# Performance work log

Hardware: AMD Instinct MI355X
Metric: run time of the kernel (lower is better)

The kernel has to match this reference:

```python
import jax, jax.numpy as jnp
import numpy as np

B, L, N, D = 128, 256, 64, 1024  # batch, text_len, img_num, feat size (text=obj=place=D)


def masked_softmax(logits, mask=None):
    # matches MaskedSoftmax(dim=1): softmax over last axis, then renormalize by mask
    dist = jax.nn.softmax(logits, axis=-1)
    if mask is None:
        return dist
    dist = dist * mask
    return dist / jnp.sum(dist, axis=-1, keepdims=True)


def setup_inputs() -> dict:
    key = jax.random.key(0)
    ks = jax.random.split(key, 32)
    s = lambda d: 1.0 / np.sqrt(d)
    inp = {
        'text_feat': jax.random.normal(ks[0], (B, D), jnp.float32),
        'text_feats': jax.random.normal(ks[1], (B, L, D), jnp.float32),
        'img_object_feat': jax.random.normal(ks[2], (B, D), jnp.float32),
        'img_object_feats': jax.random.normal(ks[3], (B, N, D), jnp.float32),
        'img_place_feat': jax.random.normal(ks[4], (B, D), jnp.float32),
        'img_place_feats': jax.random.normal(ks[5], (B, N, D), jnp.float32),
        'src_mask': (jax.random.uniform(ks[6], (B, L)) < 0.9).astype(jnp.float32).at[:, 0].set(1.0),
        # score vectors (nn.Linear(D,1,bias=False))
        'v_to': jax.random.uniform(ks[7], (D,), jnp.float32, -s(D), s(D)),
        'v_tp': jax.random.uniform(ks[8], (D,), jnp.float32, -s(D), s(D)),
        'v_io': jax.random.uniform(ks[9], (D,), jnp.float32, -s(D), s(D)),
        'v_ip': jax.random.uniform(ks[10], (D,), jnp.float32, -s(D), s(D)),
        # cross-modal projections (bias=False), torch layout [out,in]
        'W_t2o': jax.random.uniform(ks[11], (D, D), jnp.float32, -s(D), s(D)),
        'W_t2p': jax.random.uniform(ks[12], (D, D), jnp.float32, -s(D), s(D)),
        'W_o2t': jax.random.uniform(ks[13], (D, D), jnp.float32, -s(D), s(D)),
        'W_p2t': jax.random.uniform(ks[14], (D, D), jnp.float32, -s(D), s(D)),
        # self projections with bias
        'W_oo': jax.random.uniform(ks[15], (D, D), jnp.float32, -s(D), s(D)),
        'b_oo': jax.random.uniform(ks[16], (D,), jnp.float32, -s(D), s(D)),
        'W_pp': jax.random.uniform(ks[17], (D, D), jnp.float32, -s(D), s(D)),
        'b_pp': jax.random.uniform(ks[18], (D,), jnp.float32, -s(D), s(D)),
        'W_tot': jax.random.uniform(ks[19], (D, D), jnp.float32, -s(D), s(D)),
        'b_tot': jax.random.uniform(ks[20], (D,), jnp.float32, -s(D), s(D)),
        'W_tpt': jax.random.uniform(ks[21], (D, D), jnp.float32, -s(D), s(D)),
        'b_tpt': jax.random.uniform(ks[22], (D,), jnp.float32, -s(D), s(D)),
        # output linear: in = 2*D + D + D = 4D
        'W_out': jax.random.uniform(ks[23], (D, 4 * D), jnp.float32, -s(4 * D), s(4 * D)),
        'b_out': jax.random.uniform(ks[24], (D,), jnp.float32, -s(4 * D), s(4 * D)),
    }
    return inp


def _text_att_ctx(text_feat, img_feats, W_img2text, W_text, b_text, v):
    # additive attention of text over image regions
    e = jnp.tanh(jnp.einsum('bnd,td->bnt', img_feats, W_img2text)
                 + (text_feat @ W_text.T + b_text)[:, None, :])
    scores = jnp.einsum('bnt,t->bn', e, v)
    dist = masked_softmax(scores)
    return jnp.einsum('bn,bnd->bd', dist, img_feats)


def _img_att_ctx(img_feat, text_feats, W_text2img, W_img, b_img, v, mask):
    e = jnp.tanh(jnp.einsum('bld,id->bli', text_feats, W_text2img)
                 + (img_feat @ W_img.T + b_img)[:, None, :])
    scores = jnp.einsum('bli,i->bl', e, v)
    dist = masked_softmax(scores, mask)
    return jnp.einsum('bl,bld->bd', dist, text_feats)


def reference(text_feat, text_feats, img_object_feat, img_object_feats, img_place_feat,
              img_place_feats, src_mask, v_to, v_tp, v_io, v_ip, W_t2o, W_t2p, W_o2t,
              W_p2t, W_oo, b_oo, W_pp, b_pp, W_tot, b_tot, W_tpt, b_tpt, W_out, b_out):
    img_object_context = _text_att_ctx(text_feat, img_object_feats, W_o2t, W_tot, b_tot, v_to)
    img_place_context = _text_att_ctx(text_feat, img_place_feats, W_p2t, W_tpt, b_tpt, v_tp)
    text_object_context = _img_att_ctx(img_object_feat, text_feats, W_t2o, W_oo, b_oo, v_io, src_mask)
    text_place_context = _img_att_ctx(img_place_feat, text_feats, W_t2p, W_pp, b_pp, v_ip, src_mask)
    combined = jnp.concatenate([img_object_context, img_place_context,
                                text_object_context, text_place_context], axis=1)
    # dropout is identity at inference
    return combined @ W_out.T + b_out
```

## Files before the change

### kernel.cpp

```cpp
#include <hip/hip_runtime.h>
#include <hip/hip_bf16.h>

typedef __attribute__((ext_vector_type(8))) short bf16x8;
typedef __attribute__((ext_vector_type(4))) float f32x4;
typedef __attribute__((ext_vector_type(2))) long lx2;

__device__ __forceinline__ uint pack_bf16x2(float a, float b) {
    __hip_bfloat162 p = __float22bfloat162_rn(make_float2(a, b));
    union { __hip_bfloat162 h; uint u; } c; c.h = p; return c.u;
}

__device__ __forceinline__ float fast_tanh(float x) {
    float e = __expf(2.f * x);
    return 1.f - 2.f * __builtin_amdgcn_rcpf(e + 1.f);
}

__device__ __forceinline__ float wredmax(float v) {
    #pragma unroll
    for (int o = 32; o; o >>= 1) v = fmaxf(v, __shfl_xor(v, o, 64));
    return v;
}
__device__ __forceinline__ float wredsum(float v) {
    #pragma unroll
    for (int o = 32; o; o >>= 1) v += __shfl_xor(v, o, 64);
    return v;
}

__device__ __forceinline__ void gload16(const void* g, void* l) {
    __builtin_amdgcn_global_load_lds(
        (const __attribute__((address_space(1))) void*)g,
        (__attribute__((address_space(3))) void*)l, 16, 0, 0);
}

struct CvtTab {
    const float* src[8];
    ushort* dst[8];
    unsigned cum[9];
};

__global__ void cvt_bf16(CvtTab t, unsigned total4) {
    unsigned stride = gridDim.x * blockDim.x;
    for (unsigned i = blockIdx.x * blockDim.x + threadIdx.x; i < total4; i += stride) {
        int j = 0;
        while (i >= t.cum[j + 1]) ++j;
        unsigned off = i - t.cum[j];
        float4 v = reinterpret_cast<const float4*>(t.src[j])[off];
        uint2 o;
        o.x = pack_bf16x2(v.x, v.y);
        o.y = pack_bf16x2(v.z, v.w);
        reinterpret_cast<uint2*>(t.dst[j])[off] = o;
    }
}

struct Cvt8Tab {
    const float* src[8];
    uchar* dst[8];
    unsigned cum[9];
};

__device__ __forceinline__ uint pk8(float4 v) {
    int r = __builtin_amdgcn_cvt_pk_fp8_f32(v.x, v.y, 0, false);
    r = __builtin_amdgcn_cvt_pk_fp8_f32(v.z, v.w, r, true);
    return (uint)r;
}

__global__ void cvt_fp8(Cvt8Tab t, unsigned total16) {
    unsigned stride = gridDim.x * blockDim.x;
    for (unsigned i = blockIdx.x * blockDim.x + threadIdx.x; i < total16; i += stride) {
        int j = 0;
        while (i >= t.cum[j + 1]) ++j;
        unsigned o = i - t.cum[j];
        unsigned row = o >> 6, c = o & 63, tt = c >> 2, pp = c & 3;
        const float* s0 = t.src[j] + (size_t)row * 1024 + tt * 64 + pp * 8;
        float4 a0 = *(const float4*)(s0);
        float4 a1 = *(const float4*)(s0 + 4);
        float4 b0 = *(const float4*)(s0 + 32);
        float4 b1 = *(const float4*)(s0 + 36);
        uint4 ov;
        ov.x = pk8(a0); ov.y = pk8(a1); ov.z = pk8(b0); ov.w = pk8(b1);
        *reinterpret_cast<uint4*>(t.dst[j] + (size_t)o * 16) = ov;
    }
}

struct PArgs {
    const uchar* A[2];
    const uchar* Wa[2];
    const uchar* Wb[2];
    const float* qa[2];
    const float* qb[2];
    const float* va[2];
    const float* vb[2];
    float* oa[2];
    float* ob[2];
};

__global__ __launch_bounds__(512, 1) void gemm_pipe8(PArgs P, int nmul, int nbadd,
                                                     int bshift, int brshift)
{
    extern __shared__ char smem[];

    const int tid = threadIdx.x;
    const int lane = tid & 63, wv = tid >> 6;
    const int wr = wv >> 2, wc = wv & 3;
    const int lrow = lane & 15, lk = lane >> 4;

    const int br = blockIdx.x >> brshift;
    const int m0 = (blockIdx.x & ((1 << brshift) - 1)) << 8;
    const int na = blockIdx.y * nmul;
    const int nb = na + nbadd;

    const uchar* A  = P.A[br];
    const uchar* Wa = P.Wa[br];
    const uchar* Wb = P.Wb[br];

    const int rr = tid >> 2;
    const int c  = (tid & 3) ^ ((tid >> 3) & 3);
    const uchar* sA0 = A  + (size_t)(m0 + rr) * 1024 + c * 16;
    const uchar* sA1 = A  + (size_t)(m0 + 128 + rr) * 1024 + c * 16;
    const uchar* sW0 = Wa + (size_t)(na + rr) * 1024 + c * 16;
    const uchar* sW1 = Wb + (size_t)(nb + rr) * 1024 + c * 16;

    auto stage = [&](int t, int d) {
        char* b = smem + d * 32768 + tid * 16;
        size_t k = (size_t)t * 64;
        gload16(sA0 + k, b);
        gload16(sA1 + k, b + 8192);
        gload16(sW0 + k, b + 16384);
        gload16(sW1 + k, b + 24576);
    };

    auto rdA = [&](int d, int mi) -> lx2 {
        int row = wr * 128 + mi * 16 + lrow;
        return *(const lx2*)(smem + d * 32768 + row * 64 +
                             ((lk ^ ((row >> 1) & 3)) << 4));
    };
    auto rdB = [&](int d, int ni) -> lx2 {
        int row = wc * 64 + ni * 16 + lrow;
        return *(const lx2*)(smem + d * 32768 + 16384 + row * 64 +
                             ((lk ^ ((row >> 1) & 3)) << 4));
    };

    f32x4 acc[8][4];
    #pragma unroll
    for (int i = 0; i < 8; ++i)
        #pragma unroll
        for (int j = 0; j < 4; ++j) { f32x4 z = {0.f,0.f,0.f,0.f}; acc[i][j] = z; }

    stage(0, 0);
    asm volatile("s_waitcnt vmcnt(0)" ::: "memory");
    __syncthreads();

    auto body = [&](int t, int cur, int nxt, bool pf) {
        lx2 af[4], bfr[4];
        if (pf) stage(t + 1, nxt);
        #pragma unroll
        for (int ni = 0; ni < 4; ++ni) bfr[ni] = rdB(cur, ni);
        #pragma unroll
        for (int mi = 0; mi < 4; ++mi) af[mi] = rdA(cur, mi);
        __builtin_amdgcn_s_setprio(1);
        #pragma unroll
        for (int mi = 0; mi < 4; ++mi)
            #pragma unroll
            for (int ni = 0; ni < 4; ++ni) {
                acc[mi][ni] = __builtin_amdgcn_mfma_f32_16x16x32_fp8_fp8(af[mi][0], bfr[ni][0], acc[mi][ni], 0, 0, 0);
                acc[mi][ni] = __builtin_amdgcn_mfma_f32_16x16x32_fp8_fp8(af[mi][1], bfr[ni][1], acc[mi][ni], 0, 0, 0);
            }
        __builtin_amdgcn_s_setprio(0);
        #pragma unroll
        for (int mi = 0; mi < 4; ++mi) af[mi] = rdA(cur, mi + 4);
        __builtin_amdgcn_s_setprio(1);
        #pragma unroll
        for (int mi = 0; mi < 4; ++mi)
            #pragma unroll
            for (int ni = 0; ni < 4; ++ni) {
                acc[mi + 4][ni] = __builtin_amdgcn_mfma_f32_16x16x32_fp8_fp8(af[mi][0], bfr[ni][0], acc[mi + 4][ni], 0, 0, 0);
                acc[mi + 4][ni] = __builtin_amdgcn_mfma_f32_16x16x32_fp8_fp8(af[mi][1], bfr[ni][1], acc[mi + 4][ni], 0, 0, 0);
            }
        __builtin_amdgcn_s_setprio(0);
        asm volatile("s_waitcnt vmcnt(0)" ::: "memory");
        __syncthreads();
    };

    #pragma unroll 1
    for (int tt = 0; tt < 8; ++tt) {
        body(2 * tt,     0, 1, true);
        body(2 * tt + 1, 1, 0, tt < 7);
    }

    const float* qsrc = (wc < 2) ? P.qa[br] : P.qb[br];
    const float* vsrc = (wc < 2) ? P.va[br] : P.vb[br];
    float* osrc       = (wc < 2) ? P.oa[br] : P.ob[br];
    const int nbase0 = ((wc < 2) ? na : nb) + (wc & 1) * 64;
    #pragma unroll
    for (int mi = 0; mi < 8; ++mi) {
        int mbase = m0 + wr * 128 + mi * 16;
        int bb = mbase >> bshift;
        const float* qrow = qsrc + (size_t)bb * 1024;
        float part[4] = {0.f, 0.f, 0.f, 0.f};
        #pragma unroll
        for (int ni = 0; ni < 4; ++ni) {
            int nn = nbase0 + ni * 16 + lrow;
            float qn = qrow[nn], vn = vsrc[nn];
            #pragma unroll
            for (int r2 = 0; r2 < 4; ++r2)
                part[r2] += fast_tanh(acc[mi][ni][r2] + qn) * vn;
        }
        #pragma unroll
        for (int off = 1; off < 16; off <<= 1)
            #pragma unroll
            for (int r2 = 0; r2 < 4; ++r2)
                part[r2] += __shfl_xor(part[r2], off, 64);
        if (lrow == 0) {
            #pragma unroll
            for (int r2 = 0; r2 < 4; ++r2)
                atomicAdd(&osrc[mbase + lk * 4 + r2], part[r2]);
        }
    }
}

struct QArgs {
    const ushort* A[4];
    const ushort* W[4];
    const float* bias[4];
    float* out[4];
};

__global__ __launch_bounds__(256, 2) void gemm_q(QArgs Q)
{
    __shared__ char smemq[32768];
    char* As = smemq;
    char* Ws = smemq + 16384;

    const int tid = threadIdx.x;
    const int lane = tid & 63, wv = tid >> 6, wr = wv >> 1, wc = wv & 1;
    const int lrow = lane & 15, lk = lane >> 4;
    const int n0 = blockIdx.y << 7;

    const ushort* A = Q.A[blockIdx.x];
    const ushort* W = Q.W[blockIdx.x];

    f32x4 acc[4][4];
    #pragma unroll
    for (int i = 0; i < 4; ++i)
        #pragma unroll
        for (int j = 0; j < 4; ++j) { f32x4 z = {0.f,0.f,0.f,0.f}; acc[i][j] = z; }

    const int srow = tid >> 3;
    const int g = (tid & 7) ^ (srow & 7);
    const ushort* pA = A + (size_t)srow * 1024 + g * 8;
    const ushort* pW = W + (size_t)(n0 + srow) * 1024 + g * 8;

    for (int t = 0; t < 16; ++t) {
        #pragma unroll
        for (int j = 0; j < 4; ++j)
            gload16(pA + (size_t)j * 32768 + (size_t)t * 64, As + j * 4096 + tid * 16);
        #pragma unroll
        for (int j = 0; j < 4; ++j)
            gload16(pW + (size_t)j * 32768 + (size_t)t * 64, Ws + j * 4096 + tid * 16);
        __syncthreads();
        #pragma unroll
        for (int ks = 0; ks < 2; ++ks) {
            bf16x8 af[4], bfr[4];
            const int q = ks * 4 + lk;
            #pragma unroll
            for (int mi = 0; mi < 4; ++mi) {
                int row = wr * 64 + mi * 16 + lrow;
                af[mi] = *(const bf16x8*)(As + row * 128 + ((q ^ (row & 7)) << 4));
            }
            #pragma unroll
            for (int ni = 0; ni < 4; ++ni) {
                int row = wc * 64 + ni * 16 + lrow;
                bfr[ni] = *(const bf16x8*)(Ws + row * 128 + ((q ^ (row & 7)) << 4));
            }
            #pragma unroll
            for (int mi = 0; mi < 4; ++mi)
                #pragma unroll
                for (int ni = 0; ni < 4; ++ni)
                    acc[mi][ni] = __builtin_amdgcn_mfma_f32_16x16x32_bf16(af[mi], bfr[ni], acc[mi][ni], 0, 0, 0);
        }
        __syncthreads();
    }

    float* out = Q.out[blockIdx.x];
    const float* bias = Q.bias[blockIdx.x];
    #pragma unroll
    for (int mi = 0; mi < 4; ++mi) {
        int mrow0 = wr * 64 + mi * 16 + lk * 4;
        #pragma unroll
        for (int ni = 0; ni < 4; ++ni) {
            int n = n0 + wc * 64 + ni * 16 + lrow;
            float bv = bias[n];
            #pragma unroll
            for (int r = 0; r < 4; ++r)
                out[(size_t)(mrow0 + r) * 1024 + n] = acc[mi][ni][r] + bv;
        }
    }
}

__global__ __launch_bounds__(256, 2) void gemm_fin(
    const ushort* A, const ushort* W, const float* bias, float* out, int K, int kchunk)
{
    __shared__ char smemf[32768];
    char* As = smemf;
    char* Ws = smemf + 16384;

    const int tid = threadIdx.x;
    const int lane = tid & 63, wv = tid >> 6, wr = wv >> 1, wc = wv & 1;
    const int lrow = lane & 15, lk = lane >> 4;
    const int n0 = blockIdx.y << 7;
    const int nkt = kchunk >> 6;
    const int ktbase = blockIdx.z * nkt;

    f32x4 acc[4][4];
    #pragma unroll
    for (int i = 0; i < 4; ++i)
        #pragma unroll
        for (int j = 0; j < 4; ++j) { f32x4 z = {0.f,0.f,0.f,0.f}; acc[i][j] = z; }

    const int srow = tid >> 3;
    const int g = (tid & 7) ^ (srow & 7);
    const ushort* pA = A + (size_t)srow * K + ktbase * 64 + g * 8;
    const ushort* pW = W + (size_t)(n0 + srow) * K + ktbase * 64 + g * 8;

    for (int t = 0; t < nkt; ++t) {
        #pragma unroll
        for (int j = 0; j < 4; ++j)
            gload16(pA + (size_t)j * 32 * K + (size_t)t * 64, As + j * 4096 + tid * 16);
        #pragma unroll
        for (int j = 0; j < 4; ++j)
            gload16(pW + (size_t)j * 32 * K + (size_t)t * 64, Ws + j * 4096 + tid * 16);
        __syncthreads();
        #pragma unroll
        for (int ks = 0; ks < 2; ++ks) {
            bf16x8 af[4], bfr[4];
            const int q = ks * 4 + lk;
            #pragma unroll
            for (int mi = 0; mi < 4; ++mi) {
                int row = wr * 64 + mi * 16 + lrow;
                af[mi] = *(const bf16x8*)(As + row * 128 + ((q ^ (row & 7)) << 4));
            }
            #pragma unroll
            for (int ni = 0; ni < 4; ++ni) {
                int row = wc * 64 + ni * 16 + lrow;
                bfr[ni] = *(const bf16x8*)(Ws + row * 128 + ((q ^ (row & 7)) << 4));
            }
            #pragma unroll
            for (int mi = 0; mi < 4; ++mi)
                #pragma unroll
                for (int ni = 0; ni < 4; ++ni)
                    acc[mi][ni] = __builtin_amdgcn_mfma_f32_16x16x32_bf16(af[mi], bfr[ni], acc[mi][ni], 0, 0, 0);
        }
        __syncthreads();
    }

    #pragma unroll
    for (int mi = 0; mi < 4; ++mi) {
        int mrow0 = wr * 64 + mi * 16 + lk * 4;
        #pragma unroll
        for (int ni = 0; ni < 4; ++ni) {
            int n = n0 + wc * 64 + ni * 16 + lrow;
            float bv = (blockIdx.z == 0) ? bias[n] : 0.f;
            #pragma unroll
            for (int r = 0; r < 4; ++r)
                atomicAdd(&out[(size_t)(mrow0 + r) * 1024 + n], acc[mi][ni][r] + bv);
        }
    }
}

__global__ void softmax_ctx_img(const float* __restrict__ iof, const float* __restrict__ ipf,
                                const float* __restrict__ sc_io, const float* __restrict__ sc_ip,
                                ushort* __restrict__ combined)
{
    int b = blockIdx.x, br = blockIdx.y;
    const float* A  = br ? ipf : iof;
    const float* sc = br ? sc_ip : sc_io;
    __shared__ float dist[64];
    int tid = threadIdx.x;
    if (tid < 64) {
        float s  = sc[b * 64 + tid];
        float mx = wredmax(s);
        float e  = __expf(s - mx);
        float sm = wredsum(e);
        dist[tid] = e / sm;
    }
    __syncthreads();
    int d0 = tid * 4;
    float a0 = 0, a1 = 0, a2 = 0, a3 = 0;
    const float* base = A + (size_t)b * 64 * 1024 + d0;
    #pragma unroll 4
    for (int n = 0; n < 64; ++n) {
        float w = dist[n];
        float4 t = *(const float4*)(base + (size_t)n * 1024);
        a0 += w * t.x; a1 += w * t.y; a2 += w * t.z; a3 += w * t.w;
    }
    uint2 o;
    o.x = pack_bf16x2(a0, a1);
    o.y = pack_bf16x2(a2, a3);
    *(uint2*)(combined + (size_t)b * 4096 + br * 1024 + d0) = o;
}

__global__ void softmax_ctx_text(const float* __restrict__ tf,
                                 const float* __restrict__ sc_to, const float* __restrict__ sc_tp,
                                 const float* __restrict__ mask, ushort* __restrict__ combined)
{
    int b = blockIdx.x;
    __shared__ float d3[256], d4[256], red[8];
    int tid = threadIdx.x, lane = tid & 63, wv = tid >> 6;
    float s3 = sc_to[b * 256 + tid], s4 = sc_tp[b * 256 + tid], m = mask[b * 256 + tid];
    float m3 = wredmax(s3), m4 = wredmax(s4);
    if (lane == 0) { red[wv] = m3; red[4 + wv] = m4; }
    __syncthreads();
    m3 = fmaxf(fmaxf(red[0], red[1]), fmaxf(red[2], red[3]));
    m4 = fmaxf(fmaxf(red[4], red[5]), fmaxf(red[6], red[7]));
    float e3 = __expf(s3 - m3) * m, e4 = __expf(s4 - m4) * m;
    float t3 = wredsum(e3), t4 = wredsum(e4);
    __syncthreads();
    if (lane == 0) { red[wv] = t3; red[4 + wv] = t4; }
    __syncthreads();
    t3 = red[0] + red[1] + red[2] + red[3];
    t4 = red[4] + red[5] + red[6] + red[7];
    d3[tid] = e3 / t3; d4[tid] = e4 / t4;
    __syncthreads();
    int d0 = tid * 4;
    float a0 = 0, a1 = 0, a2 = 0, a3 = 0, c0 = 0, c1 = 0, c2 = 0, c3 = 0;
    const float* base = tf + (size_t)b * 256 * 1024 + d0;
    #pragma unroll 4
    for (int l = 0; l < 256; ++l) {
        float w3 = d3[l], w4 = d4[l];
        float4 t = *(const float4*)(base + (size_t)l * 1024);
        a0 += w3 * t.x; a1 += w3 * t.y; a2 += w3 * t.z; a3 += w3 * t.w;
        c0 += w4 * t.x; c1 += w4 * t.y; c2 += w4 * t.z; c3 += w4 * t.w;
    }
    uint2 o;
    o.x = pack_bf16x2(a0, a1); o.y = pack_bf16x2(a2, a3);
    *(uint2*)(combined + (size_t)b * 4096 + 2048 + d0) = o;
    o.x = pack_bf16x2(c0, c1); o.y = pack_bf16x2(c2, c3);
    *(uint2*)(combined + (size_t)b * 4096 + 3072 + d0) = o;
}

extern "C" void kernel_launch(void* const* d_in, const int* in_sizes, int n_in,
                              void* d_out, int out_size, void* d_ws, size_t ws_size,
                              hipStream_t stream) {
    const float* text_feat        = (const float*)d_in[0];
    const float* text_feats       = (const float*)d_in[1];
    const float* img_object_feat  = (const float*)d_in[2];
    const float* img_object_feats = (const float*)d_in[3];
    const float* img_place_feat   = (const float*)d_in[4];
    const float* img_place_feats  = (const float*)d_in[5];
    const float* src_mask         = (const float*)d_in[6];
    const float* v_to  = (const float*)d_in[7];
    const float* v_tp  = (const float*)d_in[8];
    const float* v_io  = (const float*)d_in[9];
    const float* v_ip  = (const float*)d_in[10];
    const float* W_t2o = (const float*)d_in[11];
    const float* W_t2p = (const float*)d_in[12];
    const float* W_o2t = (const float*)d_in[13];
    const float* W_p2t = (const float*)d_in[14];
    const float* W_oo  = (const float*)d_in[15];
    const float* b_oo  = (const float*)d_in[16];
    const float* W_pp  = (const float*)d_in[17];
    const float* b_pp  = (const float*)d_in[18];
    const float* W_tot = (const float*)d_in[19];
    const float* b_tot = (const float*)d_in[20];
    const float* W_tpt = (const float*)d_in[21];
    const float* b_tpt = (const float*)d_in[22];
    const float* W_out = (const float*)d_in[23];
    const float* b_out = (const float*)d_in[24];

    char* p = (char*)d_ws;
    auto alloc = [&](size_t bytes) { char* r = p; p += (bytes + 255) & ~(size_t)255; return r; };
    ushort* wq_oo  = (ushort*)alloc((size_t)1024 * 1024 * 2);
    ushort* wq_pp  = (ushort*)alloc((size_t)1024 * 1024 * 2);
    ushort* wq_tot = (ushort*)alloc((size_t)1024 * 1024 * 2);
    ushort* wq_tpt = (ushort*)alloc((size_t)1024 * 1024 * 2);
    ushort* wb_out = (ushort*)alloc((size_t)1024 * 4096 * 2);
    ushort* tfq_bf  = (ushort*)alloc((size_t)128 * 1024 * 2);
    ushort* iofq_bf = (ushort*)alloc((size_t)128 * 1024 * 2);
    ushort* ipfq_bf = (ushort*)alloc((size_t)128 * 1024 * 2);
    uchar* w8_t2o = (uchar*)alloc((size_t)1024 * 1024);
    uchar* w8_t2p = (uchar*)alloc((size_t)1024 * 1024);
    uchar* w8_o2t = (uchar*)alloc((size_t)1024 * 1024);
    uchar* w8_p2t = (uchar*)alloc((size_t)1024 * 1024);
    uchar* tf8  = (uchar*)alloc((size_t)32768 * 1024);
    uchar* iof8 = (uchar*)alloc((size_t)8192 * 1024);
    uchar* ipf8 = (uchar*)alloc((size_t)8192 * 1024);
    float* q_tot = (float*)alloc((size_t)128 * 1024 * 4);
    float* q_tpt = (float*)alloc((size_t)128 * 1024 * 4);
    float* q_oo  = (float*)alloc((size_t)128 * 1024 * 4);
    float* q_pp  = (float*)alloc((size_t)128 * 1024 * 4);
    float* scores = (float*)alloc((size_t)(8192 * 2 + 32768 * 2) * 4);
    float* sc_io = scores, *sc_ip = scores + 8192, *sc_to = scores + 16384, *sc_tp = scores + 49152;
    ushort* comb_bf = (ushort*)alloc((size_t)128 * 4096 * 2);

    Cvt8Tab t8;
    const float* s8[7] = { W_t2o, W_t2p, W_o2t, W_p2t, text_feats, img_object_feats, img_place_feats };
    uchar* d8[7] = { w8_t2o, w8_t2p, w8_o2t, w8_p2t, tf8, iof8, ipf8 };
    unsigned n16[7] = { 65536, 65536, 65536, 65536, 2097152, 524288, 524288 };
    unsigned cum8 = 0;
    for (int i = 0; i < 7; ++i) { t8.src[i] = s8[i]; t8.dst[i] = d8[i]; t8.cum[i] = cum8; cum8 += n16[i]; }
    t8.src[7] = nullptr; t8.dst[7] = nullptr; t8.cum[7] = cum8; t8.cum[8] = cum8;
    cvt_fp8<<<4096, 256, 0, stream>>>(t8, cum8);

    CvtTab tb;
    const float* sb[8] = { W_oo, W_pp, W_tot, W_tpt, W_out, text_feat, img_object_feat, img_place_feat };
    ushort* db[8] = { wq_oo, wq_pp, wq_tot, wq_tpt, wb_out, tfq_bf, iofq_bf, ipfq_bf };
    unsigned nb4[8] = { 262144, 262144, 262144, 262144, 1048576, 32768, 32768, 32768 };
    unsigned cumb = 0;
    for (int i = 0; i < 8; ++i) { tb.src[i] = sb[i]; tb.dst[i] = db[i]; tb.cum[i] = cumb; cumb += nb4[i]; }
    tb.cum[8] = cumb;
    cvt_bf16<<<2048, 256, 0, stream>>>(tb, cumb);

    hipMemsetAsync(scores, 0, (size_t)(8192 * 2 + 32768 * 2) * 4, stream);
    hipMemsetAsync(d_out, 0, (size_t)128 * 1024 * 4, stream);

    QArgs qa;
    qa.A[0] = tfq_bf;  qa.W[0] = wq_tot; qa.bias[0] = b_tot; qa.out[0] = q_tot;
    qa.A[1] = tfq_bf;  qa.W[1] = wq_tpt; qa.bias[1] = b_tpt; qa.out[1] = q_tpt;
    qa.A[2] = iofq_bf; qa.W[2] = wq_oo;  qa.bias[2] = b_oo;  qa.out[2] = q_oo;
    qa.A[3] = ipfq_bf; qa.W[3] = wq_pp;  qa.bias[3] = b_pp;  qa.out[3] = q_pp;
    gemm_q<<<dim3(4, 8), 256, 0, stream>>>(qa);

    PArgs pi;
    pi.A[0] = iof8;   pi.Wa[0] = w8_o2t; pi.Wb[0] = w8_o2t;
    pi.qa[0] = q_tot; pi.qb[0] = q_tot;  pi.va[0] = v_to; pi.vb[0] = v_to;
    pi.oa[0] = sc_io; pi.ob[0] = sc_io;
    pi.A[1] = ipf8;   pi.Wa[1] = w8_p2t; pi.Wb[1] = w8_p2t;
    pi.qa[1] = q_tpt; pi.qb[1] = q_tpt;  pi.va[1] = v_tp; pi.vb[1] = v_tp;
    pi.oa[1] = sc_ip; pi.ob[1] = sc_ip;
    gemm_pipe8<<<dim3(64, 4), 512, 65536, stream>>>(pi, 256, 128, 6, 5);

    PArgs pt;
    pt.A[0] = tf8;    pt.Wa[0] = w8_t2o; pt.Wb[0] = w8_t2p;
    pt.qa[0] = q_oo;  pt.qb[0] = q_pp;   pt.va[0] = v_io; pt.vb[0] = v_ip;
    pt.oa[0] = sc_to; pt.ob[0] = sc_tp;
    pt.A[1] = pt.A[0]; pt.Wa[1] = pt.Wa[0]; pt.Wb[1] = pt.Wb[0];
    pt.qa[1] = pt.qa[0]; pt.qb[1] = pt.qb[0]; pt.va[1] = pt.va[0]; pt.vb[1] = pt.vb[0];
    pt.oa[1] = pt.oa[0]; pt.ob[1] = pt.ob[0];
    gemm_pipe8<<<dim3(128, 8), 512, 65536, stream>>>(pt, 128, 0, 8, 7);

    softmax_ctx_img<<<dim3(128, 2), 256, 0, stream>>>(img_object_feats, img_place_feats, sc_io, sc_ip, comb_bf);
    softmax_ctx_text<<<dim3(128), 256, 0, stream>>>(text_feats, sc_to, sc_tp, src_mask, comb_bf);

    gemm_fin<<<dim3(1, 8, 8), 256, 0, stream>>>(comb_bf, wb_out, b_out, (float*)d_out, 4096, 512);
}
```

Before: 295.6 us.

## Merge conversion and softmax kernels, split-K the small GEMMs for more blocks

Merges the fp8 and bf16 conversion kernels into one launch, and merges the image and text softmax-context kernels into one launch that splits the text branch across two blocks per batch. Splits gemm_q along K into 4 chunks with atomic accumulation and doubles gemm_fin's split-K, so these small GEMMs launch more blocks. The one memset now clears q buffers plus scores, assuming they are allocated contiguously. This cuts launch count and raises parallelism, at the cost of extra atomics and a layout-dependent memset.

New measurement: 274.4 us. 1.08x faster.

```diff
diff --git a/kernel.cpp b/kernel.cpp
--- a/kernel.cpp
+++ b/kernel.cpp
@@ -32,53 +32,51 @@
         (__attribute__((address_space(3))) void*)l, 16, 0, 0);
 }
 
+struct Cvt8Tab {
+    const float* src[8];
+    uchar* dst[8];
+    unsigned cum[9];
+};
 struct CvtTab {
     const float* src[8];
     ushort* dst[8];
     unsigned cum[9];
 };
 
-__global__ void cvt_bf16(CvtTab t, unsigned total4) {
-    unsigned stride = gridDim.x * blockDim.x;
-    for (unsigned i = blockIdx.x * blockDim.x + threadIdx.x; i < total4; i += stride) {
-        int j = 0;
-        while (i >= t.cum[j + 1]) ++j;
-        unsigned off = i - t.cum[j];
-        float4 v = reinterpret_cast<const float4*>(t.src[j])[off];
-        uint2 o;
-        o.x = pack_bf16x2(v.x, v.y);
-        o.y = pack_bf16x2(v.z, v.w);
-        reinterpret_cast<uint2*>(t.dst[j])[off] = o;
-    }
-}
-
-struct Cvt8Tab {
-    const float* src[8];
-    uchar* dst[8];
-    unsigned cum[9];
-};
-
 __device__ __forceinline__ uint pk8(float4 v) {
     int r = __builtin_amdgcn_cvt_pk_fp8_f32(v.x, v.y, 0, false);
     r = __builtin_amdgcn_cvt_pk_fp8_f32(v.z, v.w, r, true);
     return (uint)r;
 }
 
-__global__ void cvt_fp8(Cvt8Tab t, unsigned total16) {
+__global__ void cvt_all(Cvt8Tab t8, unsigned total8, CvtTab tb, unsigned totalb) {
     unsigned stride = gridDim.x * blockDim.x;
-    for (unsigned i = blockIdx.x * blockDim.x + threadIdx.x; i < total16; i += stride) {
-        int j = 0;
-        while (i >= t.cum[j + 1]) ++j;
-        unsigned o = i - t.cum[j];
-        unsigned row = o >> 6, c = o & 63, tt = c >> 2, pp = c & 3;
-        const float* s0 = t.src[j] + (size_t)row * 1024 + tt * 64 + pp * 8;
-        float4 a0 = *(const float4*)(s0);
-        float4 a1 = *(const float4*)(s0 + 4);
-        float4 b0 = *(const float4*)(s0 + 32);
-        float4 b1 = *(const float4*)(s0 + 36);
-        uint4 ov;
-        ov.x = pk8(a0); ov.y = pk8(a1); ov.z = pk8(b0); ov.w = pk8(b1);
-        *reinterpret_cast<uint4*>(t.dst[j] + (size_t)o * 16) = ov;
+    unsigned total = total8 + totalb;
+    for (unsigned i = blockIdx.x * blockDim.x + threadIdx.x; i < total; i += stride) {
+        if (i < total8) {
+            int j = 0;
+            while (i >= t8.cum[j + 1]) ++j;
+            unsigned o = i - t8.cum[j];
+            unsigned row = o >> 6, c = o & 63, tt = c >> 2, pp = c & 3;
+            const float* s0 = t8.src[j] + (size_t)row * 1024 + tt * 64 + pp * 8;
+            float4 a0 = *(const float4*)(s0);
+            float4 a1 = *(const float4*)(s0 + 4);
+            float4 b0 = *(const float4*)(s0 + 32);
+            float4 b1 = *(const float4*)(s0 + 36);
+            uint4 ov;
+            ov.x = pk8(a0); ov.y = pk8(a1); ov.z = pk8(b0); ov.w = pk8(b1);
+            *reinterpret_cast<uint4*>(t8.dst[j] + (size_t)o * 16) = ov;
+        } else {
+            unsigned ii = i - total8;
+            int j = 0;
+            while (ii >= tb.cum[j + 1]) ++j;
+            unsigned off = ii - tb.cum[j];
+            float4 v = reinterpret_cast<const float4*>(tb.src[j])[off];
+            uint2 o;
+            o.x = pack_bf16x2(v.x, v.y);
+            o.y = pack_bf16x2(v.z, v.w);
+            reinterpret_cast<uint2*>(tb.dst[j])[off] = o;
+        }
     }
 }
 
@@ -225,7 +223,7 @@
     float* out[4];
 };
 
-__global__ __launch_bounds__(256, 2) void gemm_q(QArgs Q)
+__global__ __launch_bounds__(256, 2) void gemm_q(QArgs Q, int kchunk)
 {
     __shared__ char smemq[32768];
     char* As = smemq;
@@ -235,6 +233,8 @@
     const int lane = tid & 63, wv = tid >> 6, wr = wv >> 1, wc = wv & 1;
     const int lrow = lane & 15, lk = lane >> 4;
     const int n0 = blockIdx.y << 7;
+    const int nkt = kchunk >> 6;
+    const int ktbase = blockIdx.z * nkt;
 
     const ushort* A = Q.A[blockIdx.x];
     const ushort* W = Q.W[blockIdx.x];
@@ -247,10 +247,10 @@
 
     const int srow = tid >> 3;
     const int g = (tid & 7) ^ (srow & 7);
-    const ushort* pA = A + (size_t)srow * 1024 + g * 8;
-    const ushort* pW = W + (size_t)(n0 + srow) * 1024 + g * 8;
-
-    for (int t = 0; t < 16; ++t) {
+    const ushort* pA = A + (size_t)srow * 1024 + (size_t)ktbase * 64 + g * 8;
+    const ushort* pW = W + (size_t)(n0 + srow) * 1024 + (size_t)ktbase * 64 + g * 8;
+
+    for (int t = 0; t < nkt; ++t) {
         #pragma unroll
         for (int j = 0; j < 4; ++j)
             gload16(pA + (size_t)j * 32768 + (size_t)t * 64, As + j * 4096 + tid * 16);
@@ -289,10 +289,10 @@
         #pragma unroll
         for (int ni = 0; ni < 4; ++ni) {
             int n = n0 + wc * 64 + ni * 16 + lrow;
-            float bv = bias[n];
+            float bv = (blockIdx.z == 0) ? bias[n] : 0.f;
             #pragma unroll
             for (int r = 0; r < 4; ++r)
-                out[(size_t)(mrow0 + r) * 1024 + n] = acc[mi][ni][r] + bv;
+                atomicAdd(&out[(size_t)(mrow0 + r) * 1024 + n], acc[mi][ni][r] + bv);
         }
     }
 }
@@ -367,75 +367,70 @@
     }
 }
 
-__global__ void softmax_ctx_img(const float* __restrict__ iof, const float* __restrict__ ipf,
-                                const float* __restrict__ sc_io, const float* __restrict__ sc_ip,
-                                ushort* __restrict__ combined)
+__global__ void softmax_ctx(const float* __restrict__ tf,
+                            const float* __restrict__ iof, const float* __restrict__ ipf,
+                            const float* __restrict__ sc_to, const float* __restrict__ sc_tp,
+                            const float* __restrict__ sc_io, const float* __restrict__ sc_ip,
+                            const float* __restrict__ mask, ushort* __restrict__ combined)
 {
-    int b = blockIdx.x, br = blockIdx.y;
-    const float* A  = br ? ipf : iof;
-    const float* sc = br ? sc_ip : sc_io;
-    __shared__ float dist[64];
-    int tid = threadIdx.x;
-    if (tid < 64) {
-        float s  = sc[b * 64 + tid];
-        float mx = wredmax(s);
-        float e  = __expf(s - mx);
-        float sm = wredsum(e);
-        dist[tid] = e / sm;
-    }
-    __syncthreads();
-    int d0 = tid * 4;
-    float a0 = 0, a1 = 0, a2 = 0, a3 = 0;
-    const float* base = A + (size_t)b * 64 * 1024 + d0;
-    #pragma unroll 4
-    for (int n = 0; n < 64; ++n) {
-        float w = dist[n];
-        float4 t = *(const float4*)(base + (size_t)n * 1024);
-        a0 += w * t.x; a1 += w * t.y; a2 += w * t.z; a3 += w * t.w;
-    }
-    uint2 o;
-    o.x = pack_bf16x2(a0, a1);
-    o.y = pack_bf16x2(a2, a3);
-    *(uint2*)(combined + (size_t)b * 4096 + br * 1024 + d0) = o;
-}
-
-__global__ void softmax_ctx_text(const float* __restrict__ tf,
-                                 const float* __restrict__ sc_to, const float* __restrict__ sc_tp,
-                                 const float* __restrict__ mask, ushort* __restrict__ combined)
-{
-    int b = blockIdx.x;
-    __shared__ float d3[256], d4[256], red[8];
+    int b = blockIdx.x, y = blockIdx.y;
     int tid = threadIdx.x, lane = tid & 63, wv = tid >> 6;
-    float s3 = sc_to[b * 256 + tid], s4 = sc_tp[b * 256 + tid], m = mask[b * 256 + tid];
-    float m3 = wredmax(s3), m4 = wredmax(s4);
-    if (lane == 0) { red[wv] = m3; red[4 + wv] = m4; }
-    __syncthreads();
-    m3 = fmaxf(fmaxf(red[0], red[1]), fmaxf(red[2], red[3]));
-    m4 = fmaxf(fmaxf(red[4], red[5]), fmaxf(red[6], red[7]));
-    float e3 = __expf(s3 - m3) * m, e4 = __expf(s4 - m4) * m;
-    float t3 = wredsum(e3), t4 = wredsum(e4);
-    __syncthreads();
-    if (lane == 0) { red[wv] = t3; red[4 + wv] = t4; }
-    __syncthreads();
-    t3 = red[0] + red[1] + red[2] + red[3];
-    t4 = red[4] + red[5] + red[6] + red[7];
-    d3[tid] = e3 / t3; d4[tid] = e4 / t4;
-    __syncthreads();
-    int d0 = tid * 4;
-    float a0 = 0, a1 = 0, a2 = 0, a3 = 0, c0 = 0, c1 = 0, c2 = 0, c3 = 0;
-    const float* base = tf + (size_t)b * 256 * 1024 + d0;
-    #pragma unroll 4
-    for (int l = 0; l < 256; ++l) {
-        float w3 = d3[l], w4 = d4[l];
-        float4 t = *(const float4*)(base + (size_t)l * 1024);
-        a0 += w3 * t.x; a1 += w3 * t.y; a2 += w3 * t.z; a3 += w3 * t.w;
-        c0 += w4 * t.x; c1 += w4 * t.y; c2 += w4 * t.z; c3 += w4 * t.w;
-    }
-    uint2 o;
-    o.x = pack_bf16x2(a0, a1); o.y = pack_bf16x2(a2, a3);
-    *(uint2*)(combined + (size_t)b * 4096 + 2048 + d0) = o;
-    o.x = pack_bf16x2(c0, c1); o.y = pack_bf16x2(c2, c3);
-    *(uint2*)(combined + (size_t)b * 4096 + 3072 + d0) = o;
+    if (y >= 2) {
+        int brn = y - 2;
+        const float* A  = brn ? ipf : iof;
+        const float* sc = brn ? sc_ip : sc_io;
+        __shared__ float dist[64];
+        if (tid < 64) {
+            float s  = sc[b * 64 + tid];
+            float mx = wredmax(s);
+            float e  = __expf(s - mx);
+            float sm = wredsum(e);
+            dist[tid] = e / sm;
+        }
+        __syncthreads();
+        int d0 = tid * 4;
+        float a0 = 0, a1 = 0, a2 = 0, a3 = 0;
+        const float* base = A + (size_t)b * 64 * 1024 + d0;
+        #pragma unroll 4
+        for (int n = 0; n < 64; ++n) {
+            float w = dist[n];
+            float4 t = *(const float4*)(base + (size_t)n * 1024);
+            a0 += w * t.x; a1 += w * t.y; a2 += w * t.z; a3 += w * t.w;
+        }
+        uint2 o;
+        o.x = pack_bf16x2(a0, a1);
+        o.y = pack_bf16x2(a2, a3);
+        *(uint2*)(combined + (size_t)b * 4096 + brn * 1024 + d0) = o;
+    } else {
+        __shared__ float d3[256], d4[256], red[8];
+        float s3 = sc_to[b * 256 + tid], s4 = sc_tp[b * 256 + tid], m = mask[b * 256 + tid];
+        float m3 = wredmax(s3), m4 = wredmax(s4);
+        if (lane == 0) { red[wv] = m3; red[4 + wv] = m4; }
+        __syncthreads();
+        m3 = fmaxf(fmaxf(red[0], red[1]), fmaxf(red[2], red[3]));
+        m4 = fmaxf(fmaxf(red[4], red[5]), fmaxf(red[6], red[7]));
+        float e3 = __expf(s3 - m3) * m, e4 = __expf(s4 - m4) * m;
+        float t3 = wredsum(e3), t4 = wredsum(e4);
+        __syncthreads();
+        if (lane == 0) { red[wv] = t3; red[4 + wv] = t4; }
+        __syncthreads();
+        t3 = red[0] + red[1] + red[2] + red[3];
+        t4 = red[4] + red[5] + red[6] + red[7];
+        d3[tid] = e3 / t3; d4[tid] = e4 / t4;
+        __syncthreads();
+        int d0 = y * 512 + tid * 2;
+        float a0 = 0, a1 = 0, c0 = 0, c1 = 0;
+        const float* base = tf + (size_t)b * 256 * 1024 + d0;
+        #pragma unroll 4
+        for (int l = 0; l < 256; ++l) {
+            float w3 = d3[l], w4 = d4[l];
+            float2 t = *(const float2*)(base + (size_t)l * 1024);
+            a0 += w3 * t.x; a1 += w3 * t.y;
+            c0 += w4 * t.x; c1 += w4 * t.y;
+        }
+        *(uint*)(combined + (size_t)b * 4096 + 2048 + d0) = pack_bf16x2(a0, a1);
+        *(uint*)(combined + (size_t)b * 4096 + 3072 + d0) = pack_bf16x2(c0, c1);
+    }
 }
 
 extern "C" void kernel_launch(void* const* d_in, const int* in_sizes, int n_in,
@@ -499,7 +494,6 @@
     unsigned cum8 = 0;
     for (int i = 0; i < 7; ++i) { t8.src[i] = s8[i]; t8.dst[i] = d8[i]; t8.cum[i] = cum8; cum8 += n16[i]; }
     t8.src[7] = nullptr; t8.dst[7] = nullptr; t8.cum[7] = cum8; t8.cum[8] = cum8;
-    cvt_fp8<<<4096, 256, 0, stream>>>(t8, cum8);
 
     CvtTab tb;
     const float* sb[8] = { W_oo, W_pp, W_tot, W_tpt, W_out, text_feat, img_object_feat, img_place_feat };
@@ -508,9 +502,9 @@
     unsigned cumb = 0;
     for (int i = 0; i < 8; ++i) { tb.src[i] = sb[i]; tb.dst[i] = db[i]; tb.cum[i] = cumb; cumb += nb4[i]; }
     tb.cum[8] = cumb;
-    cvt_bf16<<<2048, 256, 0, stream>>>(tb, cumb);
-
-    hipMemsetAsync(scores, 0, (size_t)(8192 * 2 + 32768 * 2) * 4, stream);
+    cvt_all<<<4096, 256, 0, stream>>>(t8, cum8, tb, cumb);
+
+    hipMemsetAsync(q_tot, 0, (size_t)4 * 524288 + 327680, stream);
     hipMemsetAsync(d_out, 0, (size_t)128 * 1024 * 4, stream);
 
     QArgs qa;
@@ -518,7 +512,7 @@
     qa.A[1] = tfq_bf;  qa.W[1] = wq_tpt; qa.bias[1] = b_tpt; qa.out[1] = q_tpt;
     qa.A[2] = iofq_bf; qa.W[2] = wq_oo;  qa.bias[2] = b_oo;  qa.out[2] = q_oo;
     qa.A[3] = ipfq_bf; qa.W[3] = wq_pp;  qa.bias[3] = b_pp;  qa.out[3] = q_pp;
-    gemm_q<<<dim3(4, 8), 256, 0, stream>>>(qa);
+    gemm_q<<<dim3(4, 8, 4), 256, 0, stream>>>(qa, 256);
 
     PArgs pi;
     pi.A[0] = iof8;   pi.Wa[0] = w8_o2t; pi.Wb[0] = w8_o2t;
@@ -538,8 +532,9 @@
     pt.oa[1] = pt.oa[0]; pt.ob[1] = pt.ob[0];
     gemm_pipe8<<<dim3(128, 8), 512, 65536, stream>>>(pt, 128, 0, 8, 7);
 
-    softmax_ctx_img<<<dim3(128, 2), 256, 0, stream>>>(img_object_feats, img_place_feats, sc_io, sc_ip, comb_bf);
-    softmax_ctx_text<<<dim3(128), 256, 0, stream>>>(text_feats, sc_to, sc_tp, src_mask, comb_bf);
-
-    gemm_fin<<<dim3(1, 8, 8), 256, 0, stream>>>(comb_bf, wb_out, b_out, (float*)d_out, 4096, 512);
-}
+    softmax_ctx<<<dim3(128, 4), 256, 0, stream>>>(
+        text_feats, img_object_feats, img_place_feats,
+        sc_to, sc_tp, sc_io, sc_ip, src_mask, comb_bf);
+
+    gemm_fin<<<dim3(1, 8, 16), 256, 0, stream>>>(comb_bf, wb_out, b_out, (float*)d_out, 4096, 256);
+}
```
